# Performance work log

Measured on AMD Instinct MI355X. Metric: run time of the kernel, lower is better.

The kernel has to match this reference:

```python
import jax, jax.numpy as jnp
import numpy as np

ALPHA = 0.2          # LeakyReLU negative slope
ORTHO_LAMBDA = 0.01  # orthogonal regularization weight


def setup_inputs() -> dict:
    key = jax.random.key(0)
    ks = jax.random.split(key, 9)
    N, IN, OUT, NR, H = 50000, 128, 128, 64, 4
    E1, E2 = 200000, 50000
    return {
        "input": jax.random.normal(ks[0], (N, IN), jnp.float32),
        "edge": jax.random.randint(ks[1], (2, E1), 0, N),
        "edge_embed": jax.random.normal(ks[2], (E1, NR), jnp.float32),
        "edge_list_nhop": jax.random.randint(ks[3], (2, E2), 0, N),
        "edge_embed_nhop": jax.random.normal(ks[4], (E2, NR), jnp.float32),
        "proj": jax.random.normal(ks[5], (H, IN, IN), jnp.float32) / np.sqrt(IN).astype(np.float32),
        "W": jax.random.normal(ks[6], (H, OUT, 2 * IN + NR), jnp.float32) * 0.08,
        "a": jax.random.normal(ks[7], (H, 1, OUT), jnp.float32) * 0.1,
        "head_weights": jnp.ones((H,), jnp.float32),
    }


def reference(input, edge, edge_embed, edge_list_nhop, edge_embed_nhop, proj, W, a, head_weights):
    N, IN = input.shape
    H, OUT, _ = W.shape
    e = jnp.concatenate([edge, edge_list_nhop], axis=1)              # [2, E]
    emb = jnp.concatenate([edge_embed, edge_embed_nhop], axis=0)     # [E, NR]
    src, tgt = e[0], e[1]

    # per-head orthogonal projections: head_input[h] = input @ proj[h].T -> [H, N, IN]
    hin = jnp.einsum('ni,hoi->hno', input, proj)

    # edge_m = W @ concat(h_src, h_tgt, rel) without materializing the concat
    W_src, W_tgt, W_rel = W[:, :, :IN], W[:, :, IN:2 * IN], W[:, :, 2 * IN:]
    edge_m = (jnp.einsum('hei,hoi->heo', hin[:, src, :], W_src)
              + jnp.einsum('hei,hoi->heo', hin[:, tgt, :], W_tgt)
              + jnp.einsum('er,hor->heo', emb, W_rel))               # [H, E, OUT]

    scores = jnp.einsum('heo,ho->he', edge_m, a[:, 0, :])            # [H, E]
    powers = -jnp.where(scores > 0, scores, ALPHA * scores)         # -leakyrelu
    edge_e = jnp.exp(powers)                                         # [H, E]

    seg = lambda v: jax.ops.segment_sum(v, src, num_segments=N)
    e_rowsum = jnp.clip(jax.vmap(seg)(edge_e), 1e-12, None)          # [H, N]

    edge_w = edge_e[:, :, None] * edge_m                             # [H, E, OUT]
    head_out = jax.vmap(seg)(edge_w)                                 # [H, N, OUT]

    w = jax.nn.softmax(head_weights)
    out = jnp.einsum('h,hnd->nd', w, head_out)                       # [N, OUT]
    # faithful to torch: divides by the LAST head's e_rowsum (loop leakage)
    out = out / e_rowsum[-1][:, None]

    pp = jnp.einsum('hij,hkj->hik', proj, proj)                      # proj @ proj.T
    eye = jnp.eye(proj.shape[1], dtype=proj.dtype)
    orth_reg = ORTHO_LAMBDA * jnp.sum(jnp.sqrt(jnp.sum((pp - eye) ** 2, axis=(1, 2))))

    return jax.nn.elu(out), orth_reg
```

## Files before the change

kernel.cpp:

```cpp
#include <hip/hip_runtime.h>
#include <math.h>


#define NHEAD 4

typedef unsigned short u16;
typedef __attribute__((ext_vector_type(4))) unsigned short u16x4;
typedef __attribute__((ext_vector_type(8))) unsigned short u16x8;
typedef __attribute__((ext_vector_type(8))) short bf16x8;
typedef __attribute__((ext_vector_type(4))) float f32x4;

__device__ __forceinline__ float bf2f(u16 v) {
    union { unsigned u; float f; } x; x.u = ((unsigned)v) << 16; return x.f;
}
__device__ __forceinline__ u16 f2bf(float f) {
    union { float f; unsigned u; } x; x.f = f;
    const unsigned r = x.u + 0x7FFFu + ((x.u >> 16) & 1u);
    return (u16)(r >> 16);
}

__global__ __launch_bounds__(256) void k1_prep(
    const float* __restrict__ proj, const float* __restrict__ W,
    const float* __restrict__ a, const float* __restrict__ hw,
    u16* __restrict__ M_bf,
    float* __restrict__ asrc, float* __restrict__ atgt, float* __restrict__ arel,
    u16* __restrict__ WcatT_bf, float* __restrict__ wsoft,
    float* __restrict__ orth_part)
{
    __shared__ float projS[128*132];
    __shared__ float WS[32*132];
    __shared__ float tS[128];
    __shared__ float red[256];
    const int h = blockIdx.x;
    const int part = blockIdx.y;
    const int z = blockIdx.z;
    const int tid = threadIdx.x;
    if (part < 2 && z >= 4) return;
    const float* projH = proj + h*(128*128);
    const float* WH = W + h*(128*320);
    const float* aH = a + h*128;

    {
        const float4* p4 = (const float4*)projH;
        for (int idx = tid; idx < 4096; idx += 256)
            *(float4*)&projS[(idx>>5)*132 + (idx&31)*4] = p4[idx];
    }

    if (part < 2) {
        const int koff = part ? 128 : 0;
        for (int idx = tid; idx < 1024; idx += 256) {
            const int ol = idx>>5, jq = idx&31;
            *(float4*)&WS[ol*132 + jq*4] = *(const float4*)&WH[(z*32+ol)*320 + koff + jq*4];
        }
        __syncthreads();
        u16* Mout = M_bf + ((size_t)(part*4 + h))*16384;
        for (int idx = tid; idx < 1024; idx += 256) {
            const int ol = idx>>5, jq = idx&31;
            float4 acc; acc.x=0.f; acc.y=0.f; acc.z=0.f; acc.w=0.f;
            for (int i = 0; i < 128; ++i) {
                const float wv = WS[ol*132 + i];
                const float4 pv = *(const float4*)&projS[i*132 + jq*4];
                acc.x += wv*pv.x; acc.y += wv*pv.y; acc.z += wv*pv.z; acc.w += wv*pv.w;
            }
            u16x4 pk; pk.x=f2bf(acc.x); pk.y=f2bf(acc.y); pk.z=f2bf(acc.z); pk.w=f2bf(acc.w);
            *(u16x4*)&Mout[(z*32+ol)*128 + jq*4] = pk;
        }
        if (z == 0) {
            if (tid < 128) {
                float s = 0.f;
                for (int o = 0; o < 128; ++o) s += aH[o]*WH[o*320 + koff + tid];
                tS[tid] = s;
            }
            __syncthreads();
            if (tid < 128) {
                float s = 0.f;
                for (int i = 0; i < 128; ++i) s += tS[i]*projS[i*132 + tid];
                (part ? atgt : asrc)[h*128 + tid] = s;
            }
        }
    } else {
        __syncthreads();
        float local = 0.f;
        const int base = z*2048;
        for (int idx = base + tid; idx < base + 2048; idx += 256) {
            const int i = idx>>7, k = idx&127;
            if (i > k) continue;
            float s = 0.f;
            for (int q = 0; q < 32; ++q) {
                const float4 pi = *(const float4*)&projS[i*132 + q*4];
                const float4 pk = *(const float4*)&projS[k*132 + q*4];
                s += pi.x*pk.x + pi.y*pk.y + pi.z*pk.z + pi.w*pk.w;
            }
            if (i == k) { s -= 1.f; local += s*s; }
            else local += 2.f*s*s;
        }
        red[tid] = local;
        __syncthreads();
        for (int st = 128; st > 0; st >>= 1) {
            if (tid < st) red[tid] += red[tid+st];
            __syncthreads();
        }
        if (tid == 0) atomicAdd(&orth_part[h], red[0]);
        if (z == 0) {
            if (tid < 64) {
                float s = 0.f;
                for (int o = 0; o < 128; ++o) s += aH[o]*WH[o*320 + 256 + tid];
                arel[h*64 + tid] = s;
            }
            for (int idx = tid; idx < 8192; idx += 256) {
                const int r = idx & 63, o = idx >> 6;
                WcatT_bf[(size_t)o*256 + h*64 + r] = f2bf(WH[o*320 + 256 + r]);
            }
            if (h == 0 && tid == 0) {
                const float m = fmaxf(fmaxf(hw[0],hw[1]), fmaxf(hw[2],hw[3]));
                const float e0=expf(hw[0]-m), e1=expf(hw[1]-m), e2=expf(hw[2]-m), e3=expf(hw[3]-m);
                const float s = e0+e1+e2+e3;
                wsoft[0]=e0/s; wsoft[1]=e1/s; wsoft[2]=e2/s; wsoft[3]=e3/s;
            }
        }
    }
}

__global__ __launch_bounds__(256) void k0_nodes(
    const float* __restrict__ input, const float* __restrict__ asrc, const float* __restrict__ atgt,
    const int* __restrict__ edge, const int* __restrict__ nhop,
    u16* __restrict__ in_bf, float* __restrict__ s_src, float* __restrict__ s_tgt,
    int* __restrict__ deg, int N, int E1, int E2)
{
    __shared__ float aS[512], tS[512];
    const int tid = threadIdx.x;
    for (int idx = tid; idx < 512; idx += 256) { aS[idx] = asrc[idx]; tS[idx] = atgt[idx]; }
    const int t = blockIdx.x*256 + tid;
    if (t < E1 + E2) {
        const int src = (t < E1) ? edge[t] : nhop[t-E1];
        atomicAdd(&deg[src], 1);
    }
    __syncthreads();
    const int n = t;
    if (n >= N) return;
    const float4* inr = (const float4*)(input + (size_t)n*128);
    u16* ob = in_bf + (size_t)n*128;
    float ss[4] = {0.f,0.f,0.f,0.f}, st[4] = {0.f,0.f,0.f,0.f};
    for (int q = 0; q < 32; ++q) {
        const float4 v = inr[q];
        u16x4 pk; pk.x=f2bf(v.x); pk.y=f2bf(v.y); pk.z=f2bf(v.z); pk.w=f2bf(v.w);
        *(u16x4*)(ob + q*4) = pk;
        #pragma unroll
        for (int hh = 0; hh < 4; ++hh) {
            const float4 av = *(const float4*)&aS[hh*128 + q*4];
            const float4 tv = *(const float4*)&tS[hh*128 + q*4];
            ss[hh] += v.x*av.x + v.y*av.y + v.z*av.z + v.w*av.w;
            st[hh] += v.x*tv.x + v.y*tv.y + v.z*tv.z + v.w*tv.w;
        }
    }
    float4 o1; o1.x=ss[0]; o1.y=ss[1]; o1.z=ss[2]; o1.w=ss[3];
    float4 o2; o2.x=st[0]; o2.y=st[1]; o2.z=st[2]; o2.w=st[3];
    *(float4*)(s_src + (size_t)n*4) = o1;
    *(float4*)(s_tgt + (size_t)n*4) = o2;
}

__global__ __launch_bounds__(256) void k2_mfma(
    const u16* __restrict__ in_bf, const u16* __restrict__ M_bf,
    u16* __restrict__ tbl, int N)
{
    __shared__ u16 MS[16384];
    __shared__ u16 DW[4][16*136];
    const int tid = threadIdx.x;
    const int w = tid >> 6, lane = tid & 63;
    const int bid = blockIdx.x;
    const int nx = gridDim.x >> 3;
    const int swz = (bid & 7)*nx + (bid >> 3);
    const int n0 = (swz >> 3)*256;
    const int mat = swz & 7;
    const int m = lane & 15, kg = lane >> 4;

    {
        const u16* Mp = M_bf + (size_t)mat*16384;
        for (int c = tid; c < 2048; c += 256) {
            const int row = c >> 4, c16 = c & 15;
            const u16x8 v = *(const u16x8*)(Mp + row*128 + c16*8);
            *(u16x8*)((char*)MS + row*256 + ((c16*16) ^ ((row&7)<<4))) = v;
        }
    }
    __syncthreads();

    bf16x8 fa[8][4];
    #pragma unroll
    for (int nt = 0; nt < 8; ++nt) {
        const int row = nt*16 + m;
        #pragma unroll
        for (int ks = 0; ks < 4; ++ks) {
            const int c16 = ks*4 + kg;
            fa[nt][ks] = *(const bf16x8*)((const char*)MS + row*256 + ((c16*16) ^ ((row&7)<<4)));
        }
    }

    for (int sub = 0; sub < 4; ++sub) {
        const int nrow = n0 + w*64 + sub*16 + m;
        const int nclamp = (nrow < N) ? nrow : (N-1);
        bf16x8 fb[4];
        #pragma unroll
        for (int ks = 0; ks < 4; ++ks)
            fb[ks] = *(const bf16x8*)(in_bf + (size_t)nclamp*128 + ks*32 + kg*8);
        f32x4 acc[8];
        #pragma unroll
        for (int nt = 0; nt < 8; ++nt) { acc[nt][0]=0.f; acc[nt][1]=0.f; acc[nt][2]=0.f; acc[nt][3]=0.f; }
        #pragma unroll
        for (int nt = 0; nt < 8; ++nt)
            #pragma unroll
            for (int ks = 0; ks < 4; ++ks)
                acc[nt] = __builtin_amdgcn_mfma_f32_16x16x32_bf16(fa[nt][ks], fb[ks], acc[nt], 0, 0, 0);
        #pragma unroll
        for (int nt = 0; nt < 8; ++nt) {
            unsigned lo, hi;
            asm("v_cvt_pk_bf16_f32 %0, %1, %2" : "=v"(lo) : "v"(acc[nt][0]), "v"(acc[nt][1]));
            asm("v_cvt_pk_bf16_f32 %0, %1, %2" : "=v"(hi) : "v"(acc[nt][2]), "v"(acc[nt][3]));
            uint2 pk; pk.x = lo; pk.y = hi;
            *(uint2*)&DW[w][m*136 + nt*16 + kg*4] = pk;
        }
        const int nb = n0 + w*64 + sub*16;
        #pragma unroll
        for (int k = 0; k < 4; ++k) {
            const int idx = lane + k*64;
            const int row = idx >> 4, seg = idx & 15;
            const int n = nb + row;
            if (n < N) {
                const bf16x8 v = *(const bf16x8*)&DW[w][row*136 + seg*8];
                *(bf16x8*)(tbl + (size_t)n*1024 + mat*128 + seg*8) = v;
            }
        }
    }
}

__global__ __launch_bounds__(1024) void k_scanA(const int* __restrict__ deg, int* __restrict__ offsets,
                                                int* __restrict__ bsum, int* __restrict__ boff,
                                                int* __restrict__ sdone, int N, int nb)
{
    __shared__ int wsumS[16];
    __shared__ int ticketS;
    const int tid = threadIdx.x;
    const int lane = tid & 63, wid = tid >> 6;
    const int i0 = blockIdx.x*4096 + tid*4;
    int a0=0,a1=0,a2=0,a3=0;
    if (i0 + 3 < N) { const int4 t = *(const int4*)(deg + i0); a0=t.x; a1=t.y; a2=t.z; a3=t.w; }
    else { if (i0 < N) a0=deg[i0]; if (i0+1 < N) a1=deg[i0+1]; if (i0+2 < N) a2=deg[i0+2]; }
    const int s1=a0+a1, s2=s1+a2, s3=s2+a3;
    int s = s3;
    #pragma unroll
    for (int d = 1; d < 64; d <<= 1) { const int t = __shfl_up(s, d); if (lane >= d) s += t; }
    if (lane == 63) wsumS[wid] = s;
    __syncthreads();
    if (tid < 16) {
        int t = wsumS[tid];
        #pragma unroll
        for (int d = 1; d < 16; d <<= 1) { const int u = __shfl_up(t, d); if (tid >= d) t += u; }
        wsumS[tid] = t;
    }
    __syncthreads();
    const int ex = (wid ? wsumS[wid-1] : 0) + s - s3;
    if (i0 < N)     offsets[i0]   = ex;
    if (i0+1 < N)   offsets[i0+1] = ex + a0;
    if (i0+2 < N)   offsets[i0+2] = ex + s1;
    if (i0+3 < N)   offsets[i0+3] = ex + s2;
    if (tid == 0) {
        bsum[blockIdx.x] = wsumS[15];
        __threadfence();
        ticketS = atomicAdd(sdone, 1);
    }
    __syncthreads();
    if (ticketS == nb - 1 && tid < 64) {
        const int v = (tid < nb) ? atomicAdd(&bsum[tid], 0) : 0;
        int sv = v;
        #pragma unroll
        for (int d = 1; d < 64; d <<= 1) { const int t = __shfl_up(sv, d); if (tid >= d) sv += t; }
        if (tid < nb) boff[tid] = sv - v;
        if (tid == 63) offsets[N] = sv;
    }
}

__global__ __launch_bounds__(256) void k_fill2(
    const int* __restrict__ edge, const int* __restrict__ nhop,
    const float* __restrict__ emb1, const float* __restrict__ emb2,
    const float* __restrict__ s_src, const float* __restrict__ s_tgt,
    const float* __restrict__ arel,
    const int* __restrict__ offsets, const int* __restrict__ boff, int* __restrict__ cursor,
    int* __restrict__ csr_tgt, float* __restrict__ ee_perm, u16* __restrict__ emb_perm,
    int E1, int E2)
{
    const int tid = threadIdx.x;
    const int g = tid >> 4, l = tid & 15;
    const int E = E1 + E2;
    const float4 ar0 = *(const float4*)(arel + 0*64 + l*4);
    const float4 ar1 = *(const float4*)(arel + 1*64 + l*4);
    const float4 ar2 = *(const float4*)(arel + 2*64 + l*4);
    const float4 ar3 = *(const float4*)(arel + 3*64 + l*4);
    const int ebase = blockIdx.x*256;
    #pragma unroll 4
    for (int it = 0; it < 16; ++it) {
        const int e = ebase + it*16 + g;
        if (e >= E) continue;
        const float4 v = (e < E1) ? *(const float4*)(emb1 + (size_t)e*64 + l*4)
                                  : *(const float4*)(emb2 + (size_t)(e-E1)*64 + l*4);
        u16x4 pk; pk.x=f2bf(v.x); pk.y=f2bf(v.y); pk.z=f2bf(v.z); pk.w=f2bf(v.w);
        float p0 = v.x*ar0.x + v.y*ar0.y + v.z*ar0.z + v.w*ar0.w;
        float p1 = v.x*ar1.x + v.y*ar1.y + v.z*ar1.z + v.w*ar1.w;
        float p2 = v.x*ar2.x + v.y*ar2.y + v.z*ar2.z + v.w*ar2.w;
        float p3 = v.x*ar3.x + v.y*ar3.y + v.z*ar3.z + v.w*ar3.w;
        #pragma unroll
        for (int d = 1; d < 16; d <<= 1) {
            p0 += __shfl_xor(p0, d);
            p1 += __shfl_xor(p1, d);
            p2 += __shfl_xor(p2, d);
            p3 += __shfl_xor(p3, d);
        }
        int p = 0;
        if (l == 0) {
            int src, tgt;
            if (e < E1) { src = edge[e]; tgt = edge[E1+e]; }
            else { const int e2 = e-E1; src = nhop[e2]; tgt = nhop[E2+e2]; }
            const float4 s4 = *(const float4*)(s_src + (size_t)src*4);
            const float4 t4 = *(const float4*)(s_tgt + (size_t)tgt*4);
            float4 eo;
            { const float sc = s4.x+t4.x+p0; eo.x = expf(sc>0.f ? -sc : -0.2f*sc); }
            { const float sc = s4.y+t4.y+p1; eo.y = expf(sc>0.f ? -sc : -0.2f*sc); }
            { const float sc = s4.z+t4.z+p2; eo.z = expf(sc>0.f ? -sc : -0.2f*sc); }
            { const float sc = s4.w+t4.w+p3; eo.w = expf(sc>0.f ? -sc : -0.2f*sc); }
            const int pos = atomicAdd(&cursor[src], 1);
            p = offsets[src] + boff[src>>12] + pos;
            csr_tgt[p] = tgt;
            *(float4*)(ee_perm + (size_t)p*4) = eo;
        }
        p = __shfl(p, tid & 48);
        *(u16x4*)(emb_perm + (size_t)p*64 + l*4) = pk;
    }
}

__global__ __launch_bounds__(256) void k4_gather(
    const float* __restrict__ ee_perm, const int* __restrict__ offsets, const int* __restrict__ boff,
    const int* __restrict__ csr_tgt,
    const u16* __restrict__ emb_perm, const u16* __restrict__ tbl,
    const float* __restrict__ wsoft,
    u16* __restrict__ pout_bf, u16* __restrict__ semb_bf, float* __restrict__ rowsum3,
    int N)
{
    __shared__ float eeS[4][64][4];
    __shared__ int   tgS[4][64];
    const int lane = threadIdx.x & 63;
    const int wv = threadIdx.x >> 6;
    const int n = blockIdx.x*4 + wv;
    if (n >= N) return;
    const int hl = lane >> 4;
    const int hoff = hl*128 + (lane & 15)*8;

    union HT { u16x8 v; unsigned u[4]; };

    float acc[8];
    #pragma unroll
    for (int j = 0; j < 8; ++j) acc[j] = 0.f;
    float sm0=0.f, sm1=0.f, sm2=0.f, sm3=0.f;
    float rsl0=0.f, rsl1=0.f, rsl2=0.f, rsl3=0.f;

    const int start = offsets[n] + boff[n>>12];
    const int end = (n+1 == N) ? offsets[N] : (offsets[n+1] + boff[(n+1)>>12]);
    for (int cb = start; cb < end; cb += 64) {
        const int rem = end - cb;
        const int cnt = rem < 64 ? rem : 64;
        int tgtL = 0;
        float4 eeL; eeL.x=0.f; eeL.y=0.f; eeL.z=0.f; eeL.w=0.f;
        if (lane < cnt) {
            tgtL = csr_tgt[cb + lane];
            eeL  = *(const float4*)(ee_perm + (size_t)(cb + lane)*4);
        }
        rsl0 += eeL.x; rsl1 += eeL.y; rsl2 += eeL.z; rsl3 += eeL.w;
        *(float4*)&eeS[wv][lane][0] = eeL;
        tgS[wv][lane] = tgtL;
        const int cp = (cnt + 3) & ~3;

        HT zz; zz.u[0]=0u; zz.u[1]=0u; zz.u[2]=0u; zz.u[3]=0u;
        HT ht0=zz, ht1=zz, ht2=zz, ht3=zz;
        u16 em0=0, em1=0, em2=0, em3=0;
#define K4_FETCH(J, IDX) { const int tg_ = tgS[wv][IDX]; \
            ht##J.v = *(const u16x8*)(tbl + (size_t)tg_*1024 + 512 + hoff); \
            em##J = emb_perm[(size_t)(cb + (IDX))*64 + lane]; }
        if (0 < cnt) K4_FETCH(0, 0)
        if (1 < cnt) K4_FETCH(1, 1)
        if (2 < cnt) K4_FETCH(2, 2)
        if (3 < cnt) K4_FETCH(3, 3)

#define K4_STAGE(J) { \
            const float4 ee4 = *(const float4*)&eeS[wv][i+J][0]; \
            const float eh = eeS[wv][i+J][hl]; \
            _Pragma("unroll") \
            for (int p = 0; p < 4; ++p) { \
                union{unsigned u; float f;} lo_, hi_; \
                lo_.u = ht##J.u[p] << 16; hi_.u = ht##J.u[p] & 0xffff0000u; \
                acc[2*p]   += eh*lo_.f; \
                acc[2*p+1] += eh*hi_.f; \
            } \
            const float ev = bf2f(em##J); \
            sm0 += ee4.x*ev; sm1 += ee4.y*ev; sm2 += ee4.z*ev; sm3 += ee4.w*ev; \
            { const int ii = i + 4 + J; if (ii < cnt) K4_FETCH(J, ii) } }

        for (int i = 0; i < cp; i += 4) {
            K4_STAGE(0)
            K4_STAGE(1)
            K4_STAGE(2)
            K4_STAGE(3)
        }
#undef K4_STAGE
#undef K4_FETCH
    }

    #pragma unroll
    for (int d = 1; d < 64; d <<= 1) {
        rsl0 += __shfl_xor(rsl0, d);
        rsl1 += __shfl_xor(rsl1, d);
        rsl2 += __shfl_xor(rsl2, d);
        rsl3 += __shfl_xor(rsl3, d);
    }
    {
        const float rsh = (hl==0)?rsl0:(hl==1)?rsl1:(hl==2)?rsl2:rsl3;
        HT hs; hs.v = *(const u16x8*)(tbl + (size_t)n*1024 + hoff);
        #pragma unroll
        for (int p = 0; p < 4; ++p) {
            union{unsigned u; float f;} lo_, hi_;
            lo_.u = hs.u[p] << 16; hi_.u = hs.u[p] & 0xffff0000u;
            acc[2*p]   += rsh*lo_.f;
            acc[2*p+1] += rsh*hi_.f;
        }
    }
    if (lane == 0) rowsum3[n] = fmaxf(rsl3, 1e-12f);

    const float4 ws4 = *(const float4*)wsoft;
    const float wh = (hl==0)?ws4.x:(hl==1)?ws4.y:(hl==2)?ws4.z:ws4.w;
    float p[8];
    #pragma unroll
    for (int j = 0; j < 8; ++j) {
        float pv = wh*acc[j];
        pv += __shfl_xor(pv, 16);
        pv += __shfl_xor(pv, 32);
        p[j] = pv;
    }
    if (hl == 0) {
        u16 pk[8];
        #pragma unroll
        for (int j = 0; j < 8; ++j) pk[j] = f2bf(p[j]);
        *(u16x8*)(pout_bf + (size_t)n*128 + (lane & 15)*8) = *(u16x8*)pk;
    }
    u16* so = semb_bf + (size_t)n*256;
    so[lane]       = f2bf(ws4.x*sm0);
    so[64 + lane]  = f2bf(ws4.y*sm1);
    so[128 + lane] = f2bf(ws4.z*sm2);
    so[192 + lane] = f2bf(ws4.w*sm3);
}

__global__ __launch_bounds__(256) void k5_gemm(
    const u16* __restrict__ semb_bf, const u16* __restrict__ wcatT_bf,
    const u16* __restrict__ pout_bf,
    const float* __restrict__ rowsum3, const float* __restrict__ orth_part,
    float* __restrict__ out, int N)
{
    __shared__ float DS[64*132];
    const int tid = threadIdx.x;
    if (blockIdx.x == 0 && tid == 0)
        out[(size_t)N*128] = 0.01f*(sqrtf(orth_part[0])+sqrtf(orth_part[1])+sqrtf(orth_part[2])+sqrtf(orth_part[3]));
    const int w = tid >> 6, lane = tid & 63;
    const int m = lane & 15, kg = lane >> 4;
    const int n0 = blockIdx.x*64;

    bf16x8 fa[8];
    {
        int row = n0 + w*16 + m; if (row >= N) row = N-1;
        const u16* ap = semb_bf + (size_t)row*256 + kg*8;
        #pragma unroll
        for (int ks = 0; ks < 8; ++ks) fa[ks] = *(const bf16x8*)(ap + ks*32);
    }
    f32x4 acc[8];
    #pragma unroll
    for (int nt = 0; nt < 8; ++nt) { acc[nt][0]=0.f; acc[nt][1]=0.f; acc[nt][2]=0.f; acc[nt][3]=0.f; }
    #pragma unroll
    for (int nt = 0; nt < 8; ++nt) {
        const u16* bp = wcatT_bf + (size_t)(nt*16 + m)*256 + kg*8;
        #pragma unroll
        for (int ks = 0; ks < 8; ++ks) {
            const bf16x8 fb = *(const bf16x8*)(bp + ks*32);
            acc[nt] = __builtin_amdgcn_mfma_f32_16x16x32_bf16(fa[ks], fb, acc[nt], 0, 0, 0);
        }
    }
    #pragma unroll
    for (int nt = 0; nt < 8; ++nt) {
        const int o = nt*16 + m;
        const int r0 = w*16 + kg*4;
        #pragma unroll
        for (int r = 0; r < 4; ++r)
            DS[(r0+r)*132 + o] = acc[nt][r];
    }
    __syncthreads();
    for (int idx = tid; idx < 2048; idx += 256) {
        const int row = idx >> 5, q = idx & 31;
        const int n = n0 + row;
        if (n < N) {
            const float4 d = *(const float4*)&DS[row*132 + q*4];
            const u16x4 pb = *(const u16x4*)(pout_bf + (size_t)n*128 + q*4);
            const float rinv = 1.0f / rowsum3[n];
            float v0 = (bf2f(pb.x) + d.x)*rinv;
            float v1 = (bf2f(pb.y) + d.y)*rinv;
            float v2 = (bf2f(pb.z) + d.z)*rinv;
            float v3 = (bf2f(pb.w) + d.w)*rinv;
            v0 = (v0 > 0.f) ? v0 : expm1f(v0);
            v1 = (v1 > 0.f) ? v1 : expm1f(v1);
            v2 = (v2 > 0.f) ? v2 : expm1f(v2);
            v3 = (v3 > 0.f) ? v3 : expm1f(v3);
            float4 r4; r4.x=v0; r4.y=v1; r4.z=v2; r4.w=v3;
            *(float4*)(out + (size_t)n*128 + q*4) = r4;
        }
    }
}

extern "C" void kernel_launch(void* const* d_in, const int* in_sizes, int n_in,
                              void* d_out, int out_size, void* d_ws, size_t ws_size,
                              hipStream_t stream)
{
    const float* input = (const float*)d_in[0];
    const int*   edge  = (const int*)d_in[1];
    const float* emb1  = (const float*)d_in[2];
    const int*   nhop  = (const int*)d_in[3];
    const float* emb2  = (const float*)d_in[4];
    const float* proj  = (const float*)d_in[5];
    const float* W     = (const float*)d_in[6];
    const float* a     = (const float*)d_in[7];
    const float* hw    = (const float*)d_in[8];
    float* out = (float*)d_out;

    const int N  = in_sizes[0] / 128;
    const int E1 = in_sizes[1] / 2;
    const int E2 = in_sizes[3] / 2;
    const int E  = E1 + E2;
    (void)n_in; (void)out_size; (void)ws_size;

    char* wsb = (char*)d_ws;
    size_t off = 0;
    auto alloc = [&](size_t bytes) -> char* {
        char* p = wsb + off;
        off += (bytes + 255) & ~(size_t)255;
        return p;
    };
    u16*   in_bf    = (u16*)alloc((size_t)N*128*2);
    u16*   tbl      = (u16*)alloc((size_t)N*1024*2);
    u16*   semb_bf  = (u16*)alloc((size_t)N*256*2);
    u16*   pout_bf  = (u16*)alloc((size_t)N*128*2);
    u16*   emb_perm = (u16*)alloc((size_t)E*64*2);
    float* ee_perm  = (float*)alloc((size_t)E*4*4);
    int*   csr_tgt  = (int*)alloc((size_t)E*4);
    u16*   M_bf     = (u16*)alloc((size_t)8*16384*2);
    u16*   WcatT_bf = (u16*)alloc((size_t)128*256*2);
    float* asrc     = (float*)alloc(512*4);
    float* atgt     = (float*)alloc(512*4);
    float* arel     = (float*)alloc(256*4);
    float* s_src    = (float*)alloc((size_t)N*4*4);
    float* s_tgt    = (float*)alloc((size_t)N*4*4);
    float* wsoft    = (float*)alloc(4*4);
    float* rowsum3  = (float*)alloc((size_t)N*4);
    int*   offsets  = (int*)alloc((size_t)(N+1)*4);
    int*   bsum     = (int*)alloc(64*4);
    int*   boff     = (int*)alloc(64*4);
    const size_t zoff0 = off;
    float* orth_part= (float*)alloc(4*4);
    int*   deg      = (int*)alloc((size_t)N*4);
    int*   cursor   = (int*)alloc((size_t)N*4);
    int*   sdone    = (int*)alloc(4);
    const size_t zoff1 = off;

    hipMemsetAsync(wsb + zoff0, 0, zoff1 - zoff0, stream);

    const int nbScan = (N + 4095) / 4096;
    const int nx = (N + 255) / 256;
    const int nk0 = ((E > N ? E : N) + 255) / 256;

    k1_prep<<<dim3(NHEAD,3,8), dim3(256), 0, stream>>>(proj, W, a, hw, M_bf,
                                                       asrc, atgt, arel, WcatT_bf, wsoft, orth_part);
    k0_nodes<<<dim3(nk0), dim3(256), 0, stream>>>(input, asrc, atgt, edge, nhop,
                                                  in_bf, s_src, s_tgt, deg, N, E1, E2);
    k2_mfma<<<dim3(nx*8), dim3(256), 0, stream>>>(in_bf, M_bf, tbl, N);
    k_scanA<<<dim3(nbScan), dim3(1024), 0, stream>>>(deg, offsets, bsum, boff, sdone, N, nbScan);
    k_fill2<<<dim3((E+255)/256), dim3(256), 0, stream>>>(edge, nhop, emb1, emb2, s_src, s_tgt,
                                                         arel, offsets, boff, cursor,
                                                         csr_tgt, ee_perm, emb_perm, E1, E2);
    k4_gather<<<dim3((N+3)/4), dim3(256), 0, stream>>>(ee_perm, offsets, boff, csr_tgt, emb_perm,
                                                       tbl, wsoft, pout_bf, semb_bf, rowsum3, N);
    k5_gemm<<<dim3((N+63)/64), dim3(256), 0, stream>>>(semb_bf, WcatT_bf, pout_bf, rowsum3, orth_part,
                                                       out, N);
}
```

Before: 248.9 us.

## Move source-side projection term from gathered table into final GEMM

The table built by the MFMA kernel shrinks to only the four target-side projections per node, so it is half as large and takes half as many blocks. The source-node contribution (rowsum times source projection) is no longer read back in the gather kernel. Instead the final GEMM scales the bf16 input rows by softmax-weight times per-head rowsum and multiplies them by the source projection matrices with extra MFMAs. This cuts table write and read traffic at the cost of additional MFMA work and extra bf16 rounding of the scaled inputs in the final kernel.

Result: slower. 294.7 us (+18.4%).

```diff
diff --git a/kernel.cpp b/kernel.cpp
--- a/kernel.cpp
+++ b/kernel.cpp
@@ -168,14 +168,14 @@
     const int tid = threadIdx.x;
     const int w = tid >> 6, lane = tid & 63;
     const int bid = blockIdx.x;
-    const int nx = gridDim.x >> 3;
-    const int swz = (bid & 7)*nx + (bid >> 3);
-    const int n0 = (swz >> 3)*256;
-    const int mat = swz & 7;
+    const int chunk = gridDim.x >> 3;
+    const int swz = (bid & 7)*chunk + (bid >> 3);
+    const int n0 = (swz >> 2)*256;
+    const int mat = swz & 3;
     const int m = lane & 15, kg = lane >> 4;
 
     {
-        const u16* Mp = M_bf + (size_t)mat*16384;
+        const u16* Mp = M_bf + (size_t)(4 + mat)*16384;
         for (int c = tid; c < 2048; c += 256) {
             const int row = c >> 4, c16 = c & 15;
             const u16x8 v = *(const u16x8*)(Mp + row*128 + c16*8);
@@ -226,7 +226,7 @@
             const int n = nb + row;
             if (n < N) {
                 const bf16x8 v = *(const bf16x8*)&DW[w][row*136 + seg*8];
-                *(bf16x8*)(tbl + (size_t)n*1024 + mat*128 + seg*8) = v;
+                *(bf16x8*)(tbl + (size_t)n*512 + mat*128 + seg*8) = v;
             }
         }
     }
@@ -340,7 +340,7 @@
     const int* __restrict__ csr_tgt,
     const u16* __restrict__ emb_perm, const u16* __restrict__ tbl,
     const float* __restrict__ wsoft,
-    u16* __restrict__ pout_bf, u16* __restrict__ semb_bf, float* __restrict__ rowsum3,
+    u16* __restrict__ pout_bf, u16* __restrict__ semb_bf, float* __restrict__ rowsum4,
     int N)
 {
     __shared__ float eeS[4][64][4];
@@ -380,7 +380,7 @@
         HT ht0=zz, ht1=zz, ht2=zz, ht3=zz;
         u16 em0=0, em1=0, em2=0, em3=0;
 #define K4_FETCH(J, IDX) { const int tg_ = tgS[wv][IDX]; \
-            ht##J.v = *(const u16x8*)(tbl + (size_t)tg_*1024 + 512 + hoff); \
+            ht##J.v = *(const u16x8*)(tbl + (size_t)tg_*512 + hoff); \
             em##J = emb_perm[(size_t)(cb + (IDX))*64 + lane]; }
         if (0 < cnt) K4_FETCH(0, 0)
         if (1 < cnt) K4_FETCH(1, 1)
@@ -418,18 +418,10 @@
         rsl2 += __shfl_xor(rsl2, d);
         rsl3 += __shfl_xor(rsl3, d);
     }
-    {
-        const float rsh = (hl==0)?rsl0:(hl==1)?rsl1:(hl==2)?rsl2:rsl3;
-        HT hs; hs.v = *(const u16x8*)(tbl + (size_t)n*1024 + hoff);
-        #pragma unroll
-        for (int p = 0; p < 4; ++p) {
-            union{unsigned u; float f;} lo_, hi_;
-            lo_.u = hs.u[p] << 16; hi_.u = hs.u[p] & 0xffff0000u;
-            acc[2*p]   += rsh*lo_.f;
-            acc[2*p+1] += rsh*hi_.f;
-        }
-    }
-    if (lane == 0) rowsum3[n] = fmaxf(rsl3, 1e-12f);
+    if (lane == 0) {
+        float4 r4; r4.x=rsl0; r4.y=rsl1; r4.z=rsl2; r4.w=rsl3;
+        *(float4*)(rowsum4 + (size_t)n*4) = r4;
+    }
 
     const float4 ws4 = *(const float4*)wsoft;
     const float wh = (hl==0)?ws4.x:(hl==1)?ws4.y:(hl==2)?ws4.z:ws4.w;
@@ -456,8 +448,10 @@
 
 __global__ __launch_bounds__(256) void k5_gemm(
     const u16* __restrict__ semb_bf, const u16* __restrict__ wcatT_bf,
+    const u16* __restrict__ M_bf, const u16* __restrict__ in_bf,
     const u16* __restrict__ pout_bf,
-    const float* __restrict__ rowsum3, const float* __restrict__ orth_part,
+    const float* __restrict__ rowsum4, const float* __restrict__ wsoft,
+    const float* __restrict__ orth_part,
     float* __restrict__ out, int N)
 {
     __shared__ float DS[64*132];
@@ -468,24 +462,65 @@
     const int m = lane & 15, kg = lane >> 4;
     const int n0 = blockIdx.x*64;
 
+    int row = n0 + w*16 + m; if (row >= N) row = N-1;
+    const float4 ws4 = *(const float4*)wsoft;
+    const float4 rs4 = *(const float4*)(rowsum4 + (size_t)row*4);
+    const float rh[4] = {ws4.x*rs4.x, ws4.y*rs4.y, ws4.z*rs4.z, ws4.w*rs4.w};
+
     bf16x8 fa[8];
     {
-        int row = n0 + w*16 + m; if (row >= N) row = N-1;
         const u16* ap = semb_bf + (size_t)row*256 + kg*8;
         #pragma unroll
         for (int ks = 0; ks < 8; ++ks) fa[ks] = *(const bf16x8*)(ap + ks*32);
     }
+    bf16x8 fsc[4][4];
+    {
+        union IU { bf16x8 v; unsigned u[4]; };
+        IU fin[4];
+        #pragma unroll
+        for (int ksub = 0; ksub < 4; ++ksub)
+            fin[ksub].v = *(const bf16x8*)(in_bf + (size_t)row*128 + ksub*32 + kg*8);
+        #pragma unroll
+        for (int h = 0; h < 4; ++h) {
+            const float r = rh[h];
+            #pragma unroll
+            for (int ksub = 0; ksub < 4; ++ksub) {
+                IU o;
+                #pragma unroll
+                for (int p = 0; p < 4; ++p) {
+                    union{unsigned u; float f;} lo_, hi_;
+                    lo_.u = fin[ksub].u[p] << 16; hi_.u = fin[ksub].u[p] & 0xffff0000u;
+                    const float a = lo_.f*r, b = hi_.f*r;
+                    unsigned pk;
+                    asm("v_cvt_pk_bf16_f32 %0, %1, %2" : "=v"(pk) : "v"(a), "v"(b));
+                    o.u[p] = pk;
+                }
+                fsc[h][ksub] = o.v;
+            }
+        }
+    }
+
     f32x4 acc[8];
     #pragma unroll
     for (int nt = 0; nt < 8; ++nt) { acc[nt][0]=0.f; acc[nt][1]=0.f; acc[nt][2]=0.f; acc[nt][3]=0.f; }
     #pragma unroll
     for (int nt = 0; nt < 8; ++nt) {
-        const u16* bp = wcatT_bf + (size_t)(nt*16 + m)*256 + kg*8;
+        const int o = nt*16 + m;
+        const u16* bp = wcatT_bf + (size_t)o*256 + kg*8;
         #pragma unroll
         for (int ks = 0; ks < 8; ++ks) {
             const bf16x8 fb = *(const bf16x8*)(bp + ks*32);
             acc[nt] = __builtin_amdgcn_mfma_f32_16x16x32_bf16(fa[ks], fb, acc[nt], 0, 0, 0);
         }
+        #pragma unroll
+        for (int h = 0; h < 4; ++h) {
+            const u16* mp = M_bf + (size_t)h*16384 + (size_t)o*128 + kg*8;
+            #pragma unroll
+            for (int ksub = 0; ksub < 4; ++ksub) {
+                const bf16x8 fb = *(const bf16x8*)(mp + ksub*32);
+                acc[nt] = __builtin_amdgcn_mfma_f32_16x16x32_bf16(fsc[h][ksub], fb, acc[nt], 0, 0, 0);
+            }
+        }
     }
     #pragma unroll
     for (int nt = 0; nt < 8; ++nt) {
@@ -497,12 +532,12 @@
     }
     __syncthreads();
     for (int idx = tid; idx < 2048; idx += 256) {
-        const int row = idx >> 5, q = idx & 31;
-        const int n = n0 + row;
+        const int rrow = idx >> 5, q = idx & 31;
+        const int n = n0 + rrow;
         if (n < N) {
-            const float4 d = *(const float4*)&DS[row*132 + q*4];
+            const float4 d = *(const float4*)&DS[rrow*132 + q*4];
             const u16x4 pb = *(const u16x4*)(pout_bf + (size_t)n*128 + q*4);
-            const float rinv = 1.0f / rowsum3[n];
+            const float rinv = 1.0f / fmaxf(rowsum4[(size_t)n*4 + 3], 1e-12f);
             float v0 = (bf2f(pb.x) + d.x)*rinv;
             float v1 = (bf2f(pb.y) + d.y)*rinv;
             float v2 = (bf2f(pb.z) + d.z)*rinv;
@@ -546,7 +581,7 @@
         return p;
     };
     u16*   in_bf    = (u16*)alloc((size_t)N*128*2);
-    u16*   tbl      = (u16*)alloc((size_t)N*1024*2);
+    u16*   tbl      = (u16*)alloc((size_t)N*512*2);
     u16*   semb_bf  = (u16*)alloc((size_t)N*256*2);
     u16*   pout_bf  = (u16*)alloc((size_t)N*128*2);
     u16*   emb_perm = (u16*)alloc((size_t)E*64*2);
@@ -560,7 +595,7 @@
     float* s_src    = (float*)alloc((size_t)N*4*4);
     float* s_tgt    = (float*)alloc((size_t)N*4*4);
     float* wsoft    = (float*)alloc(4*4);
-    float* rowsum3  = (float*)alloc((size_t)N*4);
+    float* rowsum4  = (float*)alloc((size_t)N*4*4);
     int*   offsets  = (int*)alloc((size_t)(N+1)*4);
     int*   bsum     = (int*)alloc(64*4);
     int*   boff     = (int*)alloc(64*4);
@@ -581,13 +616,13 @@
                                                        asrc, atgt, arel, WcatT_bf, wsoft, orth_part);
     k0_nodes<<<dim3(nk0), dim3(256), 0, stream>>>(input, asrc, atgt, edge, nhop,
                                                   in_bf, s_src, s_tgt, deg, N, E1, E2);
-    k2_mfma<<<dim3(nx*8), dim3(256), 0, stream>>>(in_bf, M_bf, tbl, N);
+    k2_mfma<<<dim3(nx*4), dim3(256), 0, stream>>>(in_bf, M_bf, tbl, N);
     k_scanA<<<dim3(nbScan), dim3(1024), 0, stream>>>(deg, offsets, bsum, boff, sdone, N, nbScan);
     k_fill2<<<dim3((E+255)/256), dim3(256), 0, stream>>>(edge, nhop, emb1, emb2, s_src, s_tgt,
                                                          arel, offsets, boff, cursor,
                                                          csr_tgt, ee_perm, emb_perm, E1, E2);
     k4_gather<<<dim3((N+3)/4), dim3(256), 0, stream>>>(ee_perm, offsets, boff, csr_tgt, emb_perm,
-                                                       tbl, wsoft, pout_bf, semb_bf, rowsum3, N);
-    k5_gemm<<<dim3((N+63)/64), dim3(256), 0, stream>>>(semb_bf, WcatT_bf, pout_bf, rowsum3, orth_part,
-                                                       out, N);
-}
+                                                       tbl, wsoft, pout_bf, semb_bf, rowsum4, N);
+    k5_gemm<<<dim3((N+63)/64), dim3(256), 0, stream>>>(semb_bf, WcatT_bf, M_bf, in_bf, pout_bf,
+                                                       rowsum4, wsoft, orth_part, out, N);
+}
```
